# Kernel optimization log

Hardware: AMD Instinct MI355X
Metric: run time of the kernel (lower is better)

The kernel has to match this reference:

```python
import jax, jax.numpy as jnp
import numpy as np

B = 1024        # batch of independent network evaluations
N_IN = 1024     # num_inputs
L = 5           # topological layers
NPL = 2048      # nodes per layer
FANIN = 16      # fixed fan-in per node
N_OUT = 256     # num_outputs (last 256 nodes of last layer)


def setup_inputs() -> dict:
    key = jax.random.key(0)
    k_in, k_src, k_w, k_b = jax.random.split(key, 4)
    inputs = jax.random.normal(k_in, (B, N_IN), dtype=jnp.float32)
    # edge sources for layer l must point at previously-evaluated nodes (< N_IN + l*NPL)
    src_layers = []
    for l in range(L):
        kl = jax.random.fold_in(k_src, l)
        hi = N_IN + l * NPL
        src_layers.append(jax.random.randint(kl, (NPL, FANIN), 0, hi, dtype=jnp.int32))
    edge_src = jnp.stack(src_layers)                                   # [L, NPL, FANIN]
    edge_w = jax.random.normal(k_w, (L, NPL, FANIN), dtype=jnp.float32) * 0.1
    biases = jax.random.normal(k_b, (L, NPL), dtype=jnp.float32) * 0.1
    return {"inputs": inputs, "edge_src": edge_src, "edge_w": edge_w, "biases": biases}


def reference(inputs, edge_src, edge_w, biases):
    # vals holds node values in topological/evaluation order: [B, n_nodes_so_far]
    vals = inputs
    for l in range(L):
        gathered = vals[:, edge_src[l]]                                # [B, NPL, FANIN] irregular gather
        node_sum = jnp.einsum('bnf,nf->bn', gathered, edge_w[l]) + biases[l]
        act = jax.nn.sigmoid if l == L - 1 else jnp.tanh               # per-node activation dispatch
        vals = jnp.concatenate([vals, act(node_sum)], axis=1)
    return vals[:, -N_OUT:]                                            # output node values
```

## Files before the change

kernel.cpp:

```cpp
#include <hip/hip_runtime.h>
#include <hip/hip_fp16.h>

#define BSZ     1024
#define N_IN    1024
#define NLAYERS 5
#define NPL     2048
#define FANIN   16
#define N_OUT   256

#define VALS_ROWS   (N_IN + 4 * NPL)
#define CPB         4
#define NBLK        (BSZ / CPB)
#define ROW_B       8
#define LDS_BYTES   (VALS_ROWS * ROW_B)

union H4 { unsigned long long u; __half2 h2[2]; };

__global__ __launch_bounds__(256) void pack_edges_kernel(
    const int* __restrict__ src, const float* __restrict__ w,
    unsigned int* __restrict__ packed)
{
    int t = blockIdx.x * 256 + threadIdx.x;
    if (t >= NLAYERS * NPL) return;
    int l = t / NPL, n = t - l * NPL;
    const int*   s  = src + ((size_t)l * NPL + n) * FANIN;
    const float* ww = w   + ((size_t)l * NPL + n) * FANIN;
#pragma unroll
    for (int f = 0; f < FANIN; ++f) {
        unsigned int idx = (unsigned int)s[f];
        unsigned short hw = __half_as_ushort(__float2half(ww[f]));
        packed[((size_t)l * FANIN + f) * NPL + n] = (idx << 16) | (unsigned int)hw;
    }
}

__device__ __forceinline__ float fast_tanh(float x) {
    float t = __expf(2.0f * x);
    return 1.0f - 2.0f / (t + 1.0f);
}
__device__ __forceinline__ float fast_sigmoid(float x) {
    return 1.0f / (1.0f + __expf(-x));
}

__global__ __launch_bounds__(1024) void fused_net_kernel(
    const float* __restrict__ inputs,
    const unsigned int* __restrict__ packed,
    const float* __restrict__ biases,
    float* __restrict__ out)
{
    extern __shared__ char lds[];
    const int tid = threadIdx.x;
    const int c0  = blockIdx.x * CPB;

    {
        float v0 = inputs[(size_t)(c0 + 0) * N_IN + tid];
        float v1 = inputs[(size_t)(c0 + 1) * N_IN + tid];
        float v2 = inputs[(size_t)(c0 + 2) * N_IN + tid];
        float v3 = inputs[(size_t)(c0 + 3) * N_IN + tid];
        H4 rec;
        rec.h2[0] = __halves2half2(__float2half(v0), __float2half(v1));
        rec.h2[1] = __halves2half2(__float2half(v2), __float2half(v3));
        *reinterpret_cast<unsigned long long*>(lds + (size_t)tid * ROW_B) = rec.u;
    }
    __syncthreads();

    for (int l = 0; l < NLAYERS - 1; ++l) {
        const unsigned int* pkl = packed + (size_t)l * FANIN * NPL;
        const float* bl = biases + (size_t)l * NPL;
        const int wbase = N_IN + l * NPL;
#pragma unroll
        for (int it = 0; it < NPL / 1024; ++it) {
            const int n = it * 1024 + tid;
            unsigned int pk[FANIN];
#pragma unroll
            for (int f = 0; f < FANIN; ++f) pk[f] = pkl[f * NPL + n];
            const float bv = bl[n];
            float a0 = bv, a1 = bv, a2 = bv, a3 = bv;
#pragma unroll
            for (int f = 0; f < FANIN; ++f) {
                const unsigned int u   = pk[f];
                const unsigned int off = (u >> 16) << 3;
                H4 v;
                v.u = *reinterpret_cast<const unsigned long long*>(lds + off);
                const float wf = __half2float(
                    __ushort_as_half((unsigned short)(u & 0xffffu)));
                a0 = fmaf(__half2float(v.h2[0].x), wf, a0);
                a1 = fmaf(__half2float(v.h2[0].y), wf, a1);
                a2 = fmaf(__half2float(v.h2[1].x), wf, a2);
                a3 = fmaf(__half2float(v.h2[1].y), wf, a3);
            }
            a0 = fast_tanh(a0); a1 = fast_tanh(a1);
            a2 = fast_tanh(a2); a3 = fast_tanh(a3);
            H4 rec;
            rec.h2[0] = __halves2half2(__float2half(a0), __float2half(a1));
            rec.h2[1] = __halves2half2(__float2half(a2), __float2half(a3));
            *reinterpret_cast<unsigned long long*>(
                lds + (size_t)(wbase + n) * ROW_B) = rec.u;
        }
        __syncthreads();
    }

    if (tid < N_OUT) {
        const int n = (NPL - N_OUT) + tid;
        const unsigned int* pkl = packed + (size_t)(NLAYERS - 1) * FANIN * NPL;
        const float bv = biases[(size_t)(NLAYERS - 1) * NPL + n];
        unsigned int pk[FANIN];
#pragma unroll
        for (int f = 0; f < FANIN; ++f) pk[f] = pkl[f * NPL + n];
        float a0 = bv, a1 = bv, a2 = bv, a3 = bv;
#pragma unroll
        for (int f = 0; f < FANIN; ++f) {
            const unsigned int u   = pk[f];
            const unsigned int off = (u >> 16) << 3;
            H4 v;
            v.u = *reinterpret_cast<const unsigned long long*>(lds + off);
            const float wf = __half2float(
                __ushort_as_half((unsigned short)(u & 0xffffu)));
            a0 = fmaf(__half2float(v.h2[0].x), wf, a0);
            a1 = fmaf(__half2float(v.h2[0].y), wf, a1);
            a2 = fmaf(__half2float(v.h2[1].x), wf, a2);
            a3 = fmaf(__half2float(v.h2[1].y), wf, a3);
        }
        a0 = fast_sigmoid(a0); a1 = fast_sigmoid(a1);
        a2 = fast_sigmoid(a2); a3 = fast_sigmoid(a3);
        const int j = tid;
        out[(size_t)(c0 + 0) * N_OUT + j] = a0;
        out[(size_t)(c0 + 1) * N_OUT + j] = a1;
        out[(size_t)(c0 + 2) * N_OUT + j] = a2;
        out[(size_t)(c0 + 3) * N_OUT + j] = a3;
    }
}

extern "C" void kernel_launch(void* const* d_in, const int* in_sizes, int n_in,
                              void* d_out, int out_size, void* d_ws, size_t ws_size,
                              hipStream_t stream)
{
    const float* inputs   = (const float*)d_in[0];
    const int*   edge_src = (const int*)  d_in[1];
    const float* edge_w   = (const float*)d_in[2];
    const float* biases   = (const float*)d_in[3];
    float* out = (float*)d_out;
    unsigned int* packed = (unsigned int*)d_ws;

    pack_edges_kernel<<<(NLAYERS * NPL + 255) / 256, 256, 0, stream>>>(
        edge_src, edge_w, packed);

    fused_net_kernel<<<NBLK, 1024, LDS_BYTES, stream>>>(
        inputs, packed, biases, out);
}
```

Measured before the change: 27.28 us.

## Prefetch packed edges node-major and sort fan-in by bank to cut LDS conflicts

Result: faster. 25.97 us (-4.8%).

```diff
diff --git a/kernel.cpp b/kernel.cpp
--- a/kernel.cpp
+++ b/kernel.cpp
@@ -17,19 +17,36 @@
 union H4 { unsigned long long u; __half2 h2[2]; };
 
 __global__ __launch_bounds__(256) void pack_edges_kernel(
-    const int* __restrict__ src, const float* __restrict__ w,
+    const int* __restrict__ src, const float* __restrict__ wsrc,
     unsigned int* __restrict__ packed)
 {
     int t = blockIdx.x * 256 + threadIdx.x;
     if (t >= NLAYERS * NPL) return;
-    int l = t / NPL, n = t - l * NPL;
-    const int*   s  = src + ((size_t)l * NPL + n) * FANIN;
-    const float* ww = w   + ((size_t)l * NPL + n) * FANIN;
+    const int l = t / NPL;
+    const int n = t - l * NPL;
+    const int*   s  = src  + (size_t)t * FANIN;
+    const float* ww = wsrc + (size_t)t * FANIN;
+
+    int          key[FANIN];
+    unsigned int val[FANIN];
 #pragma unroll
     for (int f = 0; f < FANIN; ++f) {
         unsigned int idx = (unsigned int)s[f];
+        key[f] = (int)(idx & 15u);
+        unsigned int hi = (l < NLAYERS - 1) ? (idx << 3)
+                                            : idx;
         unsigned short hw = __half_as_ushort(__float2half(ww[f]));
-        packed[((size_t)l * FANIN + f) * NPL + n] = (idx << 16) | (unsigned int)hw;
+        val[f] = (hi << 16) | (unsigned int)hw;
+    }
+
+    unsigned int* dst = packed + (size_t)t * FANIN;
+#pragma unroll
+    for (int f = 0; f < FANIN; ++f) {
+        int rank = 0;
+#pragma unroll
+        for (int g = 0; g < FANIN; ++g)
+            rank += (key[g] < key[f]) || (key[g] == key[f] && g < f);
+        dst[(rank - n) & 15] = val[f];
     }
 }
 
@@ -63,22 +80,28 @@
     }
     __syncthreads();
 
+    unsigned int pkA[FANIN], pkB[FANIN];
+
+#pragma unroll
+    for (int f = 0; f < FANIN; ++f)
+        pkA[f] = packed[(size_t)tid * FANIN + f];
+
     for (int l = 0; l < NLAYERS - 1; ++l) {
-        const unsigned int* pkl = packed + (size_t)l * FANIN * NPL;
         const float* bl = biases + (size_t)l * NPL;
         const int wbase = N_IN + l * NPL;
-#pragma unroll
-        for (int it = 0; it < NPL / 1024; ++it) {
-            const int n = it * 1024 + tid;
-            unsigned int pk[FANIN];
-#pragma unroll
-            for (int f = 0; f < FANIN; ++f) pk[f] = pkl[f * NPL + n];
+
+#pragma unroll
+        for (int f = 0; f < FANIN; ++f)
+            pkB[f] = packed[((size_t)l * NPL + 1024 + tid) * FANIN + f];
+
+        {
+            const int n = tid;
             const float bv = bl[n];
             float a0 = bv, a1 = bv, a2 = bv, a3 = bv;
 #pragma unroll
             for (int f = 0; f < FANIN; ++f) {
-                const unsigned int u   = pk[f];
-                const unsigned int off = (u >> 16) << 3;
+                const unsigned int u   = pkA[f];
+                const unsigned int off = u >> 16;
                 H4 v;
                 v.u = *reinterpret_cast<const unsigned long long*>(lds + off);
                 const float wf = __half2float(
@@ -96,20 +119,53 @@
             *reinterpret_cast<unsigned long long*>(
                 lds + (size_t)(wbase + n) * ROW_B) = rec.u;
         }
+
+        if (l < NLAYERS - 2) {
+#pragma unroll
+            for (int f = 0; f < FANIN; ++f)
+                pkA[f] = packed[((size_t)(l + 1) * NPL + tid) * FANIN + f];
+        } else if (tid < N_OUT) {
+            const int n4 = NPL - N_OUT + tid;
+#pragma unroll
+            for (int f = 0; f < FANIN; ++f)
+                pkA[f] = packed[((size_t)(NLAYERS - 1) * NPL + n4) * FANIN + f];
+        }
+
+        {
+            const int n = 1024 + tid;
+            const float bv = bl[n];
+            float a0 = bv, a1 = bv, a2 = bv, a3 = bv;
+#pragma unroll
+            for (int f = 0; f < FANIN; ++f) {
+                const unsigned int u   = pkB[f];
+                const unsigned int off = u >> 16;
+                H4 v;
+                v.u = *reinterpret_cast<const unsigned long long*>(lds + off);
+                const float wf = __half2float(
+                    __ushort_as_half((unsigned short)(u & 0xffffu)));
+                a0 = fmaf(__half2float(v.h2[0].x), wf, a0);
+                a1 = fmaf(__half2float(v.h2[0].y), wf, a1);
+                a2 = fmaf(__half2float(v.h2[1].x), wf, a2);
+                a3 = fmaf(__half2float(v.h2[1].y), wf, a3);
+            }
+            a0 = fast_tanh(a0); a1 = fast_tanh(a1);
+            a2 = fast_tanh(a2); a3 = fast_tanh(a3);
+            H4 rec;
+            rec.h2[0] = __halves2half2(__float2half(a0), __float2half(a1));
+            rec.h2[1] = __halves2half2(__float2half(a2), __float2half(a3));
+            *reinterpret_cast<unsigned long long*>(
+                lds + (size_t)(wbase + n) * ROW_B) = rec.u;
+        }
         __syncthreads();
     }
 
     if (tid < N_OUT) {
-        const int n = (NPL - N_OUT) + tid;
-        const unsigned int* pkl = packed + (size_t)(NLAYERS - 1) * FANIN * NPL;
+        const int n = NPL - N_OUT + tid;
         const float bv = biases[(size_t)(NLAYERS - 1) * NPL + n];
-        unsigned int pk[FANIN];
-#pragma unroll
-        for (int f = 0; f < FANIN; ++f) pk[f] = pkl[f * NPL + n];
         float a0 = bv, a1 = bv, a2 = bv, a3 = bv;
 #pragma unroll
         for (int f = 0; f < FANIN; ++f) {
-            const unsigned int u   = pk[f];
+            const unsigned int u   = pkA[f];
             const unsigned int off = (u >> 16) << 3;
             H4 v;
             v.u = *reinterpret_cast<const unsigned long long*>(lds + off);
```
